# Kernel tuning notes

Hardware: AMD Instinct MI355X
Metric: run time of the kernel (lower is better)

The kernel has to match this reference:

```python
import jax, jax.numpy as jnp
import numpy as np

D, L, H, DK, DV = 768, 512, 12, 64, 64
EPS = 1e-6

def setup_inputs() -> dict:
    key = jax.random.key(0)
    ks = jax.random.split(key, 14)
    def xn(k, shape):
        # xavier_normal: std = sqrt(2/(fan_in+fan_out))
        std = (2.0 / (shape[0] + shape[1])) ** 0.5
        return jax.random.normal(k, shape, dtype=jnp.float32) * std
    B = 8
    return {
        "Q": jax.random.normal(ks[0], (B, L, D), dtype=jnp.float32),
        "K": jax.random.normal(ks[1], (B, L, D), dtype=jnp.float32),
        "V": jax.random.normal(ks[2], (B, L, D), dtype=jnp.float32),
        "W_q": xn(ks[3], (D, H * DK)),
        "W_k": xn(ks[4], (D, H * DK)),
        "W_v": xn(ks[5], (D, H * DV)),
        "W_pos": xn(ks[6], (L, L)),
        "W_neg": xn(ks[7], (L, L)),
        "W_o": xn(ks[8], (H * DV, D)),
        "W_o2": xn(ks[9], (H * DV, D)),
        "w1": xn(ks[10], (D, D)),
        "b1": jnp.zeros((D,), dtype=jnp.float32),
        "w2": xn(ks[11], (D, D)),
        "b2": jnp.zeros((D,), dtype=jnp.float32),
    }

def reference(Q, K, V, W_q, W_k, W_v, W_pos, W_neg, W_o, W_o2, w1, b1, w2, b2):
    B, Lq, _ = Q.shape
    q = (Q @ W_q).reshape(B, Lq, H, DK)  # [B,L,H,dk]
    k = (K @ W_k).reshape(B, Lq, H, DK)
    v = (V @ W_v).reshape(B, Lq, H, DV)
    temp = DK ** 0.5 + EPS
    QK = jnp.einsum('bqhd,bkhd->bhqk', q, k) / temp  # [B,H,L,L]
    # einsum 'bqk,kk->bqk' == multiply by diagonal of W_pos/W_neg along key axis
    dpos = jnp.diagonal(W_pos)  # [L]
    dneg = jnp.diagonal(W_neg)
    sp = jax.nn.softmax(QK * dpos, axis=-1)
    sn = -jax.nn.softmax(-(QK * dneg), axis=-1)
    Vp = jnp.einsum('bhqk,bkhd->bqhd', sp, v).reshape(B, Lq, H * DV)
    Vn = jnp.einsum('bhqk,bkhd->bqhd', sn, v).reshape(B, Lq, H * DV)
    out_pos = Vp @ W_o
    out_neg = Vn @ W_o2
    def ffn(X):
        return jax.nn.relu(X @ w1 + b1) @ w2 + b2
    X_pos = Q + out_pos
    X_neg = Q + out_neg
    return (ffn(X_pos) + X_pos, ffn(X_neg) + X_neg)
```

## Files before the change

kernel.cpp:

```cpp
#include <hip/hip_runtime.h>
#include <hip/hip_bf16.h>
#include <math.h>

typedef __bf16 bf16_t;
typedef __bf16 bf16x4 __attribute__((ext_vector_type(4)));
typedef __bf16 bf16x8 __attribute__((ext_vector_type(8)));
typedef float f32x4 __attribute__((ext_vector_type(4)));

#define MFMA16(a, b, c) __builtin_amdgcn_mfma_f32_16x16x32_bf16((a), (b), (c), 0, 0, 0)
#define EXP2F(x) __builtin_amdgcn_exp2f(x)

__device__ __forceinline__ void gll16(const void* g, void* lds) {
    __builtin_amdgcn_global_load_lds((const __attribute__((address_space(1))) void*)g,
                                     (__attribute__((address_space(3))) void*)lds, 16, 0, 0);
}

struct CvtPtrs {
    const float* src[3];
    bf16_t* dst[3];
};

__global__ __launch_bounds__(256) void convert_kernel(CvtPtrs p, int n8) {
    const float* src = p.src[blockIdx.y];
    bf16_t* dst = p.dst[blockIdx.y];
    const int i = blockIdx.x * 256 + threadIdx.x;
    if (i < n8) {
        const float4 u = ((const float4*)src)[i * 2];
        const float4 v = ((const float4*)src)[i * 2 + 1];
        bf16x8 o;
        o[0] = (bf16_t)u.x; o[1] = (bf16_t)u.y; o[2] = (bf16_t)u.z; o[3] = (bf16_t)u.w;
        o[4] = (bf16_t)v.x; o[5] = (bf16_t)v.y; o[6] = (bf16_t)v.z; o[7] = (bf16_t)v.w;
        ((bf16x8*)dst)[i] = o;
    }
}

struct WPtrs {
    const float* src[7];
    bf16_t* dst[7];
};

__global__ __launch_bounds__(256) void transpose_w_kernel(WPtrs p) {
    __shared__ float t[32][33];
    const float* src = p.src[blockIdx.z];
    bf16_t* dst = p.dst[blockIdx.z];
    const int tx = threadIdx.x, ty = threadIdx.y;
    const int x = blockIdx.x * 32 + tx;
    const int y0 = blockIdx.y * 32;
#pragma unroll
    for (int j = 0; j < 4; ++j)
        t[ty + j * 8][tx] = src[(size_t)(y0 + ty + j * 8) * 768 + x];
    __syncthreads();
    const int ox = blockIdx.y * 32 + tx;
    const int oy0 = blockIdx.x * 32;
#pragma unroll
    for (int j = 0; j < 4; ++j)
        dst[(size_t)(oy0 + ty + j * 8) * 768 + ox] = (bf16_t)t[tx][ty + j * 8];
}

struct GemmB {
    const bf16_t* A[3];
    const bf16_t* Bt[3];
    const float* bias;
    const float* Res[3];
    const bf16_t* ResB[3];
    float* Cf[3];
    bf16_t* Cb[3];
    bf16_t* VtOut;
};

template <bool HAS_BIAS, bool RELU, int RESMODE, int OUTMODE, bool VTZ = false>
__global__ __launch_bounds__(256, 3) void gemm2(GemmB p, int M, int K, int N) {
    __shared__ __align__(16) bf16_t As[128 * 64];
    __shared__ __align__(16) bf16_t Bs[128 * 64];
    const int z = blockIdx.z;
    const bf16_t* __restrict__ A = p.A[z];
    const bf16_t* __restrict__ Bt = p.Bt[z];
    const int tid = threadIdx.x, w = tid >> 6, l = tid & 63, l16 = l & 15, lk = l >> 4;
    const int wr = w >> 1, wc = w & 1;

    const int gx = gridDim.x, nwg = gx * gridDim.y;
    int flat = blockIdx.x + gx * blockIdx.y;
    if ((nwg & 7) == 0) flat = (flat & 7) * (nwg >> 3) + (flat >> 3);
    const int row0 = (flat / gx) * 128, col0 = (flat % gx) * 128;
    f32x4 acc[4][4] = {};

    const int lofs = w * 1024 + l * 16;
    size_t aEl[4], bEl[4];
#pragma unroll
    for (int i = 0; i < 4; ++i) {
        const int off = i * 4096 + lofs;
        const int row = off >> 7;
        const int ch = ((off >> 4) & 7) ^ (row & 7);
        aEl[i] = (size_t)(row0 + row) * K + ch * 8;
        bEl[i] = (size_t)(col0 + row) * K + ch * 8;
    }

    for (int k0 = 0; k0 < K; k0 += 64) {
        __syncthreads();
#pragma unroll
        for (int i = 0; i < 4; ++i)
            gll16(A + aEl[i] + k0, (char*)As + i * 4096 + w * 1024);
#pragma unroll
        for (int i = 0; i < 4; ++i)
            gll16(Bt + bEl[i] + k0, (char*)Bs + i * 4096 + w * 1024);
        __syncthreads();

#pragma unroll
        for (int kk = 0; kk < 2; ++kk) {
            bf16x8 af[4], bfr[4];
#pragma unroll
            for (int mt = 0; mt < 4; ++mt) {
                const int ar = wr * 64 + mt * 16 + l16;
                af[mt] = *(const bf16x8*)((const char*)As + ar * 128 +
                                          (((kk * 4 + lk) ^ (ar & 7)) << 4));
            }
#pragma unroll
            for (int nt = 0; nt < 4; ++nt) {
                const int br = wc * 64 + nt * 16 + l16;
                bfr[nt] = *(const bf16x8*)((const char*)Bs + br * 128 +
                                           (((kk * 4 + lk) ^ (br & 7)) << 4));
            }
#pragma unroll
            for (int mt = 0; mt < 4; ++mt)
#pragma unroll
                for (int nt = 0; nt < 4; ++nt)
                    acc[mt][nt] = MFMA16(af[mt], bfr[nt], acc[mt][nt]);
        }
    }

    if constexpr (VTZ) {
        if (z == 2) {
            const int b = row0 >> 9;
            const int lb0 = (row0 & 511) + wr * 64;
#pragma unroll
            for (int mt = 0; mt < 4; ++mt)
#pragma unroll
                for (int nt = 0; nt < 4; ++nt) {
                    const int col = col0 + wc * 64 + nt * 16 + l16;
                    const int hh = col >> 6, dd = col & 63;
                    bf16x4 v;
#pragma unroll
                    for (int i = 0; i < 4; ++i) v[i] = (bf16_t)acc[mt][nt][i];
                    const size_t o =
                        (((size_t)(b * 12 + hh) * 64 + dd) << 9) + lb0 + mt * 16 + lk * 4;
                    *(bf16x4*)(p.VtOut + o) = v;
                }
            return;
        }
    }

#pragma unroll
    for (int mt = 0; mt < 4; ++mt)
#pragma unroll
        for (int nt = 0; nt < 4; ++nt)
#pragma unroll
            for (int i = 0; i < 4; ++i) {
                const int row = row0 + wr * 64 + mt * 16 + lk * 4 + i;
                const int col = col0 + wc * 64 + nt * 16 + l16;
                float val = acc[mt][nt][i];
                if constexpr (HAS_BIAS) val += p.bias[col];
                if constexpr (RELU) val = fmaxf(val, 0.0f);
                const size_t o = (size_t)row * N + col;
                if constexpr (RESMODE == 1) val += p.Res[z][o];
                if constexpr (RESMODE == 2) val += (float)p.ResB[z][o];
                if constexpr (OUTMODE == 0) p.Cf[z][o] = val;
                else p.Cb[z][o] = (bf16_t)val;
            }
}

__global__ __launch_bounds__(256, 3) void attn_kernel(const bf16_t* __restrict__ qb,
                                                      const bf16_t* __restrict__ kb,
                                                      const bf16_t* __restrict__ Vt,
                                                      const float* __restrict__ Wpos,
                                                      const float* __restrict__ Wneg,
                                                      bf16_t* __restrict__ Vpb,
                                                      bf16_t* __restrict__ Vnb) {
    __shared__ __align__(16) bf16_t Ks[2][64 * 64];
    __shared__ __align__(16) bf16_t Vs[2][64 * 64];
    __shared__ __align__(16) bf16_t Ps[4][16][72];
    const int tid = threadIdx.x, w = tid >> 6, l = tid & 63, l16 = l & 15, lk = l >> 4;
    const int rg = w >> 1, sgn = w & 1;
    const int bh = blockIdx.x, qt = blockIdx.y, b = bh / 12, h = bh % 12;
    const int q0 = qt * 32 + rg * 16;
    const float SC = 1.4426950408889634f / (8.0f + 1e-6f);
    const float sc = sgn ? -SC : SC;
    const float* __restrict__ Wd = sgn ? Wneg : Wpos;

    const size_t qbase = ((size_t)(b * 512 + q0)) * 768 + h * 64;
    const bf16x8 qf0 = *(const bf16x8*)(qb + qbase + (size_t)l16 * 768 + lk * 8);
    const bf16x8 qf1 = *(const bf16x8*)(qb + qbase + (size_t)l16 * 768 + 32 + lk * 8);

    const size_t kbase0 = ((size_t)b * 512) * 768 + h * 64;
    const size_t vtb = (size_t)bh * 64 * 512;
    size_t kEl[2], vEl[2];
    int seg[2];
#pragma unroll
    for (int i = 0; i < 2; ++i) {
        seg[i] = w * 2 + i;
        const int off = seg[i] * 1024 + l * 16;
        const int row = off >> 7, slot = (off >> 4) & 7;
        kEl[i] = (size_t)row * 768 + (size_t)((slot ^ (row & 7)) * 8);
        vEl[i] = (size_t)row * 512 + (size_t)((slot ^ (row & 7)) * 8);
    }

    auto stage = [&](int c, int buf) {
#pragma unroll
        for (int i = 0; i < 2; ++i) {
            gll16(kb + kbase0 + (size_t)c * 64 * 768 + kEl[i], (char*)&Ks[buf][0] + seg[i] * 1024);
            gll16(Vt + vtb + (size_t)c * 64 + vEl[i], (char*)&Vs[buf][0] + seg[i] * 1024);
        }
    };

    f32x4 pacc[4] = {};
    float sm[4] = {0, 0, 0, 0};

    stage(0, 0);
    __syncthreads();

    for (int c = 0; c < 8; ++c) {
        const int buf = c & 1;
        if (c < 7) stage(c + 1, buf ^ 1);

        float dv[4];
#pragma unroll
        for (int nt = 0; nt < 4; ++nt)
            dv[nt] = Wd[(size_t)(c * 64 + nt * 16 + l16) * 513] * sc;

        f32x4 sacc[4] = {};
        __builtin_amdgcn_s_setprio(1);
#pragma unroll
        for (int nt = 0; nt < 4; ++nt) {
            const int kr = nt * 16 + l16;
            const bf16x8 kv0 =
                *(const bf16x8*)((const char*)&Ks[buf][0] + kr * 128 + ((lk ^ (kr & 7)) << 4));
            const bf16x8 kv1 =
                *(const bf16x8*)((const char*)&Ks[buf][0] + kr * 128 + (((4 + lk) ^ (kr & 7)) << 4));
            sacc[nt] = MFMA16(qf0, kv0, sacc[nt]);
            sacc[nt] = MFMA16(qf1, kv1, sacc[nt]);
        }
        __builtin_amdgcn_s_setprio(0);

#pragma unroll
        for (int nt = 0; nt < 4; ++nt)
#pragma unroll
            for (int i = 0; i < 4; ++i) {
                const float e = EXP2F(sacc[nt][i] * dv[nt]);
                Ps[w][lk * 4 + i][nt * 16 + l16] = (bf16_t)e;
                sm[i] += e;
            }

        __builtin_amdgcn_s_setprio(1);
#pragma unroll
        for (int kt = 0; kt < 2; ++kt) {
            const bf16x8 pa = *(const bf16x8*)&Ps[w][l16][kt * 32 + lk * 8];
#pragma unroll
            for (int nd = 0; nd < 4; ++nd) {
                const int dr = nd * 16 + l16;
                const bf16x8 vv = *(const bf16x8*)((const char*)&Vs[buf][0] + dr * 128 +
                                                   (((kt * 4 + lk) ^ (dr & 7)) << 4));
                pacc[nd] = MFMA16(pa, vv, pacc[nd]);
            }
        }
        __builtin_amdgcn_s_setprio(0);

        if (c < 7) __syncthreads();
    }

#pragma unroll
    for (int off = 1; off < 16; off <<= 1)
#pragma unroll
        for (int i = 0; i < 4; ++i) sm[i] += __shfl_xor(sm[i], off, 64);

    bf16_t* __restrict__ Out = sgn ? Vnb : Vpb;
#pragma unroll
    for (int i = 0; i < 4; ++i) {
        const float r = (sgn ? -1.0f : 1.0f) / sm[i];
        const size_t o = ((size_t)(b * 512 + q0 + lk * 4 + i)) * 768 + h * 64;
#pragma unroll
        for (int nd = 0; nd < 4; ++nd) Out[o + nd * 16 + l16] = (bf16_t)(pacc[nd][i] * r);
    }
}

extern "C" void kernel_launch(void* const* d_in, const int* in_sizes, int n_in,
                              void* d_out, int out_size, void* d_ws, size_t ws_size,
                              hipStream_t stream) {
    const float* Q = (const float*)d_in[0];
    const float* K = (const float*)d_in[1];
    const float* V = (const float*)d_in[2];
    const float* W_q = (const float*)d_in[3];
    const float* W_k = (const float*)d_in[4];
    const float* W_v = (const float*)d_in[5];
    const float* Wpos = (const float*)d_in[6];
    const float* Wneg = (const float*)d_in[7];
    const float* W_o = (const float*)d_in[8];
    const float* W_o2 = (const float*)d_in[9];
    const float* w1 = (const float*)d_in[10];
    const float* b1 = (const float*)d_in[11];
    const float* w2 = (const float*)d_in[12];
    const float* b2 = (const float*)d_in[13];
    float* out = (float*)d_out;

    char* ws = (char*)d_ws;
    const size_t act_b = (size_t)4096 * 768 * 2;
    bf16_t* Qb = (bf16_t*)(ws + 0 * act_b);
    bf16_t* Kb = (bf16_t*)(ws + 1 * act_b);
    bf16_t* Vb = (bf16_t*)(ws + 2 * act_b);
    bf16_t* Xb2 = (bf16_t*)(ws + 3 * act_b);
    bf16_t* qb = (bf16_t*)(ws + 4 * act_b);
    bf16_t* kb = (bf16_t*)(ws + 5 * act_b);
    bf16_t* Vt = (bf16_t*)(ws + 6 * act_b);
    bf16_t* Wt[7];
    for (int i = 0; i < 7; ++i) Wt[i] = (bf16_t*)(ws + 7 * act_b + (size_t)i * 768 * 768 * 2);
    bf16_t* Vpb = Qb;
    bf16_t* Vnb = Kb;
    bf16_t* Xb = Vb;
    bf16_t* Hb = qb;
    (void)Xb2;

    CvtPtrs cp;
    cp.src[0] = Q; cp.src[1] = K; cp.src[2] = V;
    cp.dst[0] = Qb; cp.dst[1] = Kb; cp.dst[2] = Vb;
    convert_kernel<<<dim3(1536, 3), 256, 0, stream>>>(cp, 393216);

    WPtrs wp;
    wp.src[0] = W_q; wp.src[1] = W_k; wp.src[2] = W_v;
    wp.src[3] = W_o; wp.src[4] = W_o2; wp.src[5] = w1; wp.src[6] = w2;
    for (int i = 0; i < 7; ++i) wp.dst[i] = Wt[i];
    transpose_w_kernel<<<dim3(24, 24, 7), dim3(32, 8), 0, stream>>>(wp);

    {
        GemmB g = {};
        g.A[0] = Qb; g.A[1] = Kb; g.A[2] = Vb;
        g.Bt[0] = Wt[0]; g.Bt[1] = Wt[1]; g.Bt[2] = Wt[2];
        g.Cb[0] = qb; g.Cb[1] = kb;
        g.VtOut = Vt;
        gemm2<false, false, 0, 1, true><<<dim3(6, 32, 3), 256, 0, stream>>>(g, 4096, 768, 768);
    }

    attn_kernel<<<dim3(96, 16), 256, 0, stream>>>(qb, kb, Vt, Wpos, Wneg, Vpb, Vnb);

    {
        GemmB g = {};
        g.A[0] = Vpb; g.A[1] = Vnb;
        g.Bt[0] = Wt[3]; g.Bt[1] = Wt[4];
        g.Res[0] = Q; g.Res[1] = Q;
        g.Cb[0] = Xb; g.Cb[1] = Xb + (size_t)4096 * 768;
        gemm2<false, false, 1, 1><<<dim3(6, 32, 2), 256, 0, stream>>>(g, 4096, 768, 768);
    }

    {
        GemmB g = {};
        g.A[0] = Xb;
        g.Bt[0] = Wt[5];
        g.bias = b1;
        g.Cb[0] = Hb;
        gemm2<true, true, 0, 1><<<dim3(6, 64, 1), 256, 0, stream>>>(g, 8192, 768, 768);
    }

    {
        GemmB g = {};
        g.A[0] = Hb;
        g.Bt[0] = Wt[6];
        g.bias = b2;
        g.ResB[0] = Xb;
        g.Cf[0] = out;
        gemm2<true, false, 2, 0><<<dim3(6, 64, 1), 256, 0, stream>>>(g, 8192, 768, 768);
    }
}
```

Measured before the change: 133.0 us.

## Use 128x96 GEMM tiles and merge convert/transpose into one prep kernel

```diff
diff --git a/kernel.cpp b/kernel.cpp
--- a/kernel.cpp
+++ b/kernel.cpp
@@ -15,46 +15,42 @@
                                      (__attribute__((address_space(3))) void*)lds, 16, 0, 0);
 }
 
-struct CvtPtrs {
-    const float* src[3];
-    bf16_t* dst[3];
+struct PrepPtrs {
+    const float* csrc[3];
+    bf16_t* cdst[3];
+    const float* wsrc[7];
+    bf16_t* wdst[7];
 };
 
-__global__ __launch_bounds__(256) void convert_kernel(CvtPtrs p, int n8) {
-    const float* src = p.src[blockIdx.y];
-    bf16_t* dst = p.dst[blockIdx.y];
-    const int i = blockIdx.x * 256 + threadIdx.x;
-    if (i < n8) {
-        const float4 u = ((const float4*)src)[i * 2];
-        const float4 v = ((const float4*)src)[i * 2 + 1];
+__global__ __launch_bounds__(256) void prep_kernel(PrepPtrs p) {
+    const int bx = blockIdx.x, tid = threadIdx.x;
+    if (bx < 4608) {
+        const int t = bx / 1536, i = (bx - t * 1536) * 256 + tid;
+        const float4 u = ((const float4*)p.csrc[t])[i * 2];
+        const float4 v = ((const float4*)p.csrc[t])[i * 2 + 1];
         bf16x8 o;
         o[0] = (bf16_t)u.x; o[1] = (bf16_t)u.y; o[2] = (bf16_t)u.z; o[3] = (bf16_t)u.w;
         o[4] = (bf16_t)v.x; o[5] = (bf16_t)v.y; o[6] = (bf16_t)v.z; o[7] = (bf16_t)v.w;
-        ((bf16x8*)dst)[i] = o;
-    }
-}
-
-struct WPtrs {
-    const float* src[7];
-    bf16_t* dst[7];
-};
-
-__global__ __launch_bounds__(256) void transpose_w_kernel(WPtrs p) {
-    __shared__ float t[32][33];
-    const float* src = p.src[blockIdx.z];
-    bf16_t* dst = p.dst[blockIdx.z];
-    const int tx = threadIdx.x, ty = threadIdx.y;
-    const int x = blockIdx.x * 32 + tx;
-    const int y0 = blockIdx.y * 32;
-#pragma unroll
-    for (int j = 0; j < 4; ++j)
-        t[ty + j * 8][tx] = src[(size_t)(y0 + ty + j * 8) * 768 + x];
-    __syncthreads();
-    const int ox = blockIdx.y * 32 + tx;
-    const int oy0 = blockIdx.x * 32;
-#pragma unroll
-    for (int j = 0; j < 4; ++j)
-        dst[(size_t)(oy0 + ty + j * 8) * 768 + ox] = (bf16_t)t[tx][ty + j * 8];
+        ((bf16x8*)p.cdst[t])[i] = o;
+    } else {
+        __shared__ float t[32][33];
+        const int q = bx - 4608, wz = q / 576, rem = q - wz * 576;
+        const int bxx = rem % 24, byy = rem / 24;
+        const float* src = p.wsrc[wz];
+        bf16_t* dst = p.wdst[wz];
+        const int tx = tid & 31, ty = tid >> 5;
+        const int x = bxx * 32 + tx;
+        const int y0 = byy * 32;
+#pragma unroll
+        for (int j = 0; j < 4; ++j)
+            t[ty + j * 8][tx] = src[(size_t)(y0 + ty + j * 8) * 768 + x];
+        __syncthreads();
+        const int ox = byy * 32 + tx;
+        const int oy0 = bxx * 32;
+#pragma unroll
+        for (int j = 0; j < 4; ++j)
+            dst[(size_t)(oy0 + ty + j * 8) * 768 + ox] = (bf16_t)t[tx][ty + j * 8];
+    }
 }
 
 struct GemmB {
@@ -71,7 +67,7 @@
 template <bool HAS_BIAS, bool RELU, int RESMODE, int OUTMODE, bool VTZ = false>
 __global__ __launch_bounds__(256, 3) void gemm2(GemmB p, int M, int K, int N) {
     __shared__ __align__(16) bf16_t As[128 * 64];
-    __shared__ __align__(16) bf16_t Bs[128 * 64];
+    __shared__ __align__(16) bf16_t Bs[96 * 64];
     const int z = blockIdx.z;
     const bf16_t* __restrict__ A = p.A[z];
     const bf16_t* __restrict__ Bt = p.Bt[z];
@@ -80,18 +76,24 @@
 
     const int gx = gridDim.x, nwg = gx * gridDim.y;
     int flat = blockIdx.x + gx * blockIdx.y;
-    if ((nwg & 7) == 0) flat = (flat & 7) * (nwg >> 3) + (flat >> 3);
-    const int row0 = (flat / gx) * 128, col0 = (flat % gx) * 128;
-    f32x4 acc[4][4] = {};
-
-    const int lofs = w * 1024 + l * 16;
-    size_t aEl[4], bEl[4];
+    flat = (flat & 7) * (nwg >> 3) + (flat >> 3);
+    const int row0 = (flat / gx) * 128, col0 = (flat % gx) * 96;
+    f32x4 acc[4][3] = {};
+
+    const int lofs = l * 16;
+    size_t aEl[4], bEl[3];
 #pragma unroll
     for (int i = 0; i < 4; ++i) {
-        const int off = i * 4096 + lofs;
+        const int off = (w * 4 + i) * 1024 + lofs;
         const int row = off >> 7;
         const int ch = ((off >> 4) & 7) ^ (row & 7);
         aEl[i] = (size_t)(row0 + row) * K + ch * 8;
+    }
+#pragma unroll
+    for (int i = 0; i < 3; ++i) {
+        const int off = (w * 3 + i) * 1024 + lofs;
+        const int row = off >> 7;
+        const int ch = ((off >> 4) & 7) ^ (row & 7);
         bEl[i] = (size_t)(col0 + row) * K + ch * 8;
     }
 
@@ -99,15 +101,15 @@
         __syncthreads();
 #pragma unroll
         for (int i = 0; i < 4; ++i)
-            gll16(A + aEl[i] + k0, (char*)As + i * 4096 + w * 1024);
-#pragma unroll
-        for (int i = 0; i < 4; ++i)
-            gll16(Bt + bEl[i] + k0, (char*)Bs + i * 4096 + w * 1024);
+            gll16(A + aEl[i] + k0, (char*)As + (w * 4 + i) * 1024);
+#pragma unroll
+        for (int i = 0; i < 3; ++i)
+            gll16(Bt + bEl[i] + k0, (char*)Bs + (w * 3 + i) * 1024);
         __syncthreads();
 
 #pragma unroll
         for (int kk = 0; kk < 2; ++kk) {
-            bf16x8 af[4], bfr[4];
+            bf16x8 af[4], bfr[3];
 #pragma unroll
             for (int mt = 0; mt < 4; ++mt) {
                 const int ar = wr * 64 + mt * 16 + l16;
@@ -115,15 +117,15 @@
                                           (((kk * 4 + lk) ^ (ar & 7)) << 4));
             }
 #pragma unroll
-            for (int nt = 0; nt < 4; ++nt) {
-                const int br = wc * 64 + nt * 16 + l16;
+            for (int nt = 0; nt < 3; ++nt) {
+                const int br = wc * 48 + nt * 16 + l16;
                 bfr[nt] = *(const bf16x8*)((const char*)Bs + br * 128 +
                                            (((kk * 4 + lk) ^ (br & 7)) << 4));
             }
 #pragma unroll
             for (int mt = 0; mt < 4; ++mt)
 #pragma unroll
-                for (int nt = 0; nt < 4; ++nt)
+                for (int nt = 0; nt < 3; ++nt)
                     acc[mt][nt] = MFMA16(af[mt], bfr[nt], acc[mt][nt]);
         }
     }
@@ -135,8 +137,8 @@
 #pragma unroll
             for (int mt = 0; mt < 4; ++mt)
 #pragma unroll
-                for (int nt = 0; nt < 4; ++nt) {
-                    const int col = col0 + wc * 64 + nt * 16 + l16;
+                for (int nt = 0; nt < 3; ++nt) {
+                    const int col = col0 + wc * 48 + nt * 16 + l16;
                     const int hh = col >> 6, dd = col & 63;
                     bf16x4 v;
 #pragma unroll
@@ -152,11 +154,11 @@
 #pragma unroll
     for (int mt = 0; mt < 4; ++mt)
 #pragma unroll
-        for (int nt = 0; nt < 4; ++nt)
+        for (int nt = 0; nt < 3; ++nt)
 #pragma unroll
             for (int i = 0; i < 4; ++i) {
                 const int row = row0 + wr * 64 + mt * 16 + lk * 4 + i;
-                const int col = col0 + wc * 64 + nt * 16 + l16;
+                const int col = col0 + wc * 48 + nt * 16 + l16;
                 float val = acc[mt][nt][i];
                 if constexpr (HAS_BIAS) val += p.bias[col];
                 if constexpr (RELU) val = fmaxf(val, 0.0f);
@@ -305,7 +307,6 @@
     bf16_t* Qb = (bf16_t*)(ws + 0 * act_b);
     bf16_t* Kb = (bf16_t*)(ws + 1 * act_b);
     bf16_t* Vb = (bf16_t*)(ws + 2 * act_b);
-    bf16_t* Xb2 = (bf16_t*)(ws + 3 * act_b);
     bf16_t* qb = (bf16_t*)(ws + 4 * act_b);
     bf16_t* kb = (bf16_t*)(ws + 5 * act_b);
     bf16_t* Vt = (bf16_t*)(ws + 6 * act_b);
@@ -315,18 +316,14 @@
     bf16_t* Vnb = Kb;
     bf16_t* Xb = Vb;
     bf16_t* Hb = qb;
-    (void)Xb2;
-
-    CvtPtrs cp;
-    cp.src[0] = Q; cp.src[1] = K; cp.src[2] = V;
-    cp.dst[0] = Qb; cp.dst[1] = Kb; cp.dst[2] = Vb;
-    convert_kernel<<<dim3(1536, 3), 256, 0, stream>>>(cp, 393216);
-
-    WPtrs wp;
-    wp.src[0] = W_q; wp.src[1] = W_k; wp.src[2] = W_v;
-    wp.src[3] = W_o; wp.src[4] = W_o2; wp.src[5] = w1; wp.src[6] = w2;
-    for (int i = 0; i < 7; ++i) wp.dst[i] = Wt[i];
-    transpose_w_kernel<<<dim3(24, 24, 7), dim3(32, 8), 0, stream>>>(wp);
+
+    PrepPtrs pp;
+    pp.csrc[0] = Q; pp.csrc[1] = K; pp.csrc[2] = V;
+    pp.cdst[0] = Qb; pp.cdst[1] = Kb; pp.cdst[2] = Vb;
+    pp.wsrc[0] = W_q; pp.wsrc[1] = W_k; pp.wsrc[2] = W_v;
+    pp.wsrc[3] = W_o; pp.wsrc[4] = W_o2; pp.wsrc[5] = w1; pp.wsrc[6] = w2;
+    for (int i = 0; i < 7; ++i) pp.wdst[i] = Wt[i];
+    prep_kernel<<<8640, 256, 0, stream>>>(pp);
 
     {
         GemmB g = {};
@@ -334,7 +331,7 @@
         g.Bt[0] = Wt[0]; g.Bt[1] = Wt[1]; g.Bt[2] = Wt[2];
         g.Cb[0] = qb; g.Cb[1] = kb;
         g.VtOut = Vt;
-        gemm2<false, false, 0, 1, true><<<dim3(6, 32, 3), 256, 0, stream>>>(g, 4096, 768, 768);
+        gemm2<false, false, 0, 1, true><<<dim3(8, 32, 3), 256, 0, stream>>>(g, 4096, 768, 768);
     }
 
     attn_kernel<<<dim3(96, 16), 256, 0, stream>>>(qb, kb, Vt, Wpos, Wneg, Vpb, Vnb);
@@ -345,7 +342,7 @@
         g.Bt[0] = Wt[3]; g.Bt[1] = Wt[4];
         g.Res[0] = Q; g.Res[1] = Q;
         g.Cb[0] = Xb; g.Cb[1] = Xb + (size_t)4096 * 768;
-        gemm2<false, false, 1, 1><<<dim3(6, 32, 2), 256, 0, stream>>>(g, 4096, 768, 768);
+        gemm2<false, false, 1, 1><<<dim3(8, 32, 2), 256, 0, stream>>>(g, 4096, 768, 768);
     }
 
     {
@@ -354,7 +351,7 @@
         g.Bt[0] = Wt[5];
         g.bias = b1;
         g.Cb[0] = Hb;
-        gemm2<true, true, 0, 1><<<dim3(6, 64, 1), 256, 0, stream>>>(g, 8192, 768, 768);
+        gemm2<true, true, 0, 1><<<dim3(8, 64, 1), 256, 0, stream>>>(g, 8192, 768, 768);
     }
 
     {
@@ -364,6 +361,6 @@
         g.bias = b2;
         g.ResB[0] = Xb;
         g.Cf[0] = out;
-        gemm2<true, false, 2, 0><<<dim3(6, 64, 1), 256, 0, stream>>>(g, 8192, 768, 768);
-    }
-}
+        gemm2<true, false, 2, 0><<<dim3(8, 64, 1), 256, 0, stream>>>(g, 8192, 768, 768);
+    }
+}
```

Result: faster. 128.3 us (-3.6%).
